# Kernel optimization log

Hardware: AMD Instinct MI355X
Metric: run time of the kernel (lower is better)

## Reference

```python
import jax, jax.numpy as jnp
import numpy as np

NUM_HEADS = 16

def setup_inputs() -> dict:
    key = jax.random.key(0)
    k1, k2, k3 = jax.random.split(key, 3)
    B, N, C = 4, 1024, 1024
    x = jax.random.normal(k1, (B, N, C), dtype=jnp.float32)
    w_qkv = jax.random.normal(k2, (C, 3 * C), dtype=jnp.float32) * (C ** -0.5)
    b_qkv = jnp.zeros((3 * C,), dtype=jnp.float32)
    w_proj = jax.random.normal(k3, (C, C), dtype=jnp.float32) * (C ** -0.5)
    b_proj = jnp.zeros((C,), dtype=jnp.float32)
    return {"x": x, "w_qkv": w_qkv, "b_qkv": b_qkv, "w_proj": w_proj, "b_proj": b_proj}

def reference(x, w_qkv, b_qkv, w_proj, b_proj):
    B, N, C = x.shape
    H = NUM_HEADS
    D = C // H
    scale = D ** -0.5
    # qkv projection: [B,N,3C] -> [3,B,H,N,D]
    qkv = (x @ w_qkv + b_qkv).reshape(B, N, 3, H, D).transpose(2, 0, 3, 1, 4)
    q, k, v = qkv[0], qkv[1], qkv[2]
    q = q * scale
    attn = jnp.einsum('bhnd,bhmd->bhnm', q, k)  # full N x N scores
    attn = jax.nn.softmax(attn, axis=-1)
    out = jnp.einsum('bhnm,bhmd->bhnd', attn, v)  # [B,H,N,D]
    out = out.transpose(0, 2, 1, 3).reshape(B, N, C)
    return out @ w_proj + b_proj
```

## Files before the change

kernel.cpp:

```cpp
#include <hip/hip_runtime.h>

typedef unsigned short u16;
typedef unsigned int u32;
typedef __attribute__((ext_vector_type(8))) short bf16x8;
typedef __attribute__((ext_vector_type(4))) float f32x4;
typedef __attribute__((ext_vector_type(16))) float f32x16;

#define LOG2E 1.4426950408889634f
#define QSCALE (0.125f * LOG2E)

__device__ __forceinline__ u16 f2bf(float f) {
  union { float f; u32 u; } x; x.f = f;
  u32 r = x.u + 0x7fffu + ((x.u >> 16) & 1u);
  return (u16)(r >> 16);
}

__device__ __forceinline__ u32 cvtpk(float a, float b) {
  u32 r;
  asm("v_cvt_pk_bf16_f32 %0, %1, %2" : "=v"(r) : "v"(a), "v"(b));
  return r;
}

__device__ __forceinline__ bf16x8 mkfrag(u32 a, u32 b, u32 c, u32 d) {
  union { u32 w[4]; bf16x8 v; } u;
  u.w[0] = a; u.w[1] = b; u.w[2] = c; u.w[3] = d;
  return u.v;
}

__device__ __forceinline__ void gload_lds16(const void* g, void* l) {
  __builtin_amdgcn_global_load_lds((const __attribute__((address_space(1))) u32*)g,
                                   (__attribute__((address_space(3))) u32*)l, 16, 0, 0);
}

__device__ __forceinline__ void packP(const f32x16& s, int hi, bf16x8& P0, bf16x8& P1) {
  u32 w0 = cvtpk(s[0], s[1]),  w1 = cvtpk(s[2], s[3]);
  u32 w2 = cvtpk(s[4], s[5]),  w3 = cvtpk(s[6], s[7]);
  u32 w4 = cvtpk(s[8], s[9]),  w5 = cvtpk(s[10], s[11]);
  u32 w6 = cvtpk(s[12], s[13]), w7 = cvtpk(s[14], s[15]);
  u32 x0 = __shfl_xor((int)w0, 32), x1 = __shfl_xor((int)w1, 32);
  u32 x2 = __shfl_xor((int)w2, 32), x3 = __shfl_xor((int)w3, 32);
  u32 x4 = __shfl_xor((int)w4, 32), x5 = __shfl_xor((int)w5, 32);
  u32 x6 = __shfl_xor((int)w6, 32), x7 = __shfl_xor((int)w7, 32);
  P0 = mkfrag(hi ? x2 : w0, hi ? x3 : w1, hi ? w2 : x0, hi ? w3 : x1);
  P1 = mkfrag(hi ? x6 : w4, hi ? x7 : w5, hi ? w6 : x4, hi ? w7 : x5);
}

__global__ __launch_bounds__(256) void k_cvt_x(const float* __restrict__ in, u16* __restrict__ out) {
  int i = blockIdx.x * 256 + threadIdx.x;
  const float4* p = (const float4*)in;
  float4 a = p[i * 2], b = p[i * 2 + 1];
  uint4 o;
  o.x = (u32)f2bf(a.x) | ((u32)f2bf(a.y) << 16);
  o.y = (u32)f2bf(a.z) | ((u32)f2bf(a.w) << 16);
  o.z = (u32)f2bf(b.x) | ((u32)f2bf(b.y) << 16);
  o.w = (u32)f2bf(b.z) | ((u32)f2bf(b.w) << 16);
  ((uint4*)out)[i] = o;
}

__global__ __launch_bounds__(256) void k_transpose_cvt(const float* __restrict__ src, u16* __restrict__ dst,
                                                       int R, int Cc) {
  __shared__ float tile[32][33];
  int c0 = blockIdx.x * 32, r0 = blockIdx.y * 32;
  int tx = threadIdx.x, ty = threadIdx.y;
  #pragma unroll
  for (int j = 0; j < 4; ++j)
    tile[ty * 4 + j][tx] = src[(r0 + ty * 4 + j) * Cc + c0 + tx];
  __syncthreads();
  #pragma unroll
  for (int j = 0; j < 4; ++j) {
    int cl = ty * 4 + j;
    dst[(c0 + cl) * R + r0 + tx] = f2bf(tile[tx][cl]);
  }
}

template <int EPI, int NBN>
__global__ __launch_bounds__(512) void k_gemm(const u16* __restrict__ A, const u16* __restrict__ Bt,
                                              const float* __restrict__ bias,
                                              u16* __restrict__ oq, u16* __restrict__ ok,
                                              u16* __restrict__ ovt, float* __restrict__ of) {
  __shared__ u16 lds[24576];
  const int tid = threadIdx.x;
  const int l = tid & 63, w = tid >> 6;
  const int wm = w >> 2, wn = w & 3;
  const int lr = l & 15, lh = l >> 4;
  const int cpx = gridDim.x >> 3;
  const int wg = (blockIdx.x & 7) * cpx + (blockIdx.x >> 3);
  const int bn = wg % NBN, bm = wg / NBN;

  f32x4 acc[4][2] = {};
  const int e = tid * 8;
  const int srow = e >> 5;
  const int sgr  = (e >> 3) & 3;
  const int scol = (sgr ^ ((srow >> 1) & 3)) * 8;
  const u16* gA = A + (bm * 128 + srow) * 1024 + scol;
  const u16* gB = Bt + (bn * 128 + srow) * 1024 + scol;

  #define GSTAGE(kk, b)                                              \
    do {                                                             \
      gload_lds16(gA + (kk), lds + (b) * 8192 + e);                  \
      gload_lds16(gB + (kk), lds + (b) * 8192 + 4096 + e);           \
    } while (0)

  GSTAGE(0, 0);
  GSTAGE(32, 1);
  int cur = 0, nxt = 2;

  for (int it = 0; it < 32; ++it) {
    if (it < 31) asm volatile("s_waitcnt vmcnt(2)" ::: "memory");
    else         asm volatile("s_waitcnt vmcnt(0)" ::: "memory");
    __builtin_amdgcn_s_barrier();
    __builtin_amdgcn_sched_barrier(0);

    if (it < 30) GSTAGE((it + 2) * 32, nxt);

    const u16* Asc = lds + cur * 8192;
    bf16x8 af[4], bfr[2];
    #pragma unroll
    for (int mi = 0; mi < 4; ++mi) {
      int r = wm * 64 + mi * 16 + lr;
      af[mi] = *(const bf16x8*)(Asc + r * 32 + ((lh ^ ((r >> 1) & 3)) * 8));
    }
    #pragma unroll
    for (int ni = 0; ni < 2; ++ni) {
      int r = wn * 32 + ni * 16 + lr;
      bfr[ni] = *(const bf16x8*)(Asc + 4096 + r * 32 + ((lh ^ ((r >> 1) & 3)) * 8));
    }
    #pragma unroll
    for (int mi = 0; mi < 4; ++mi)
      #pragma unroll
      for (int ni = 0; ni < 2; ++ni)
        acc[mi][ni] = __builtin_amdgcn_mfma_f32_16x16x32_bf16(af[mi], bfr[ni], acc[mi][ni], 0, 0, 0);

    cur = (cur == 2) ? 0 : cur + 1;
    nxt = (nxt == 2) ? 0 : nxt + 1;
  }
  #undef GSTAGE

  if (EPI == 0) {
    #pragma unroll
    for (int ni = 0; ni < 2; ++ni) {
      int col = bn * 128 + wn * 32 + ni * 16 + lr;
      float bb = bias[col];
      #pragma unroll
      for (int mi = 0; mi < 4; ++mi) {
        int row = bm * 128 + wm * 64 + mi * 16 + lh * 4;
        #pragma unroll
        for (int r = 0; r < 4; ++r)
          of[(row + r) * (NBN * 128) + col] = acc[mi][ni][r] + bb;
      }
    }
  } else {
    const int s = bn >> 3;
    __syncthreads();
    if (s < 2) {
      u16* dst = (s == 0) ? oq : ok;
      const float sc = (s == 0) ? QSCALE : 1.0f;
      #pragma unroll
      for (int ni = 0; ni < 2; ++ni) {
        int cl = wn * 32 + ni * 16 + lr;
        float bb = bias[bn * 128 + cl];
        #pragma unroll
        for (int mi = 0; mi < 4; ++mi) {
          int rl = wm * 64 + mi * 16 + lh * 4;
          #pragma unroll
          for (int r = 0; r < 4; ++r)
            lds[(rl + r) * 136 + cl] = f2bf((acc[mi][ni][r] + bb) * sc);
        }
      }
      __syncthreads();
      const int row = tid >> 2, q4 = tid & 3;
      const int h0 = ((bn * 128) & 1023) >> 6;
      const int b = (bm * 128) >> 10, n0 = (bm * 128) & 1023;
      const u16* srow2 = lds + row * 136 + q4 * 32;
      u16* drow = dst + ((u32)((b * 16 + h0 + (q4 >> 1)) * 1024) + n0 + row) * 64 + (q4 & 1) * 32;
      #pragma unroll
      for (int j = 0; j < 4; ++j)
        *(uint4*)(drow + j * 8) = *(const uint4*)(srow2 + j * 8);
    } else {
      #pragma unroll
      for (int ni = 0; ni < 2; ++ni) {
        int cl = wn * 32 + ni * 16 + lr;
        float bb = bias[bn * 128 + cl];
        #pragma unroll
        for (int mi = 0; mi < 4; ++mi) {
          int rl = wm * 64 + mi * 16 + lh * 4;
          u32 p0 = (u32)f2bf(acc[mi][ni][0] + bb) | ((u32)f2bf(acc[mi][ni][1] + bb) << 16);
          u32 p1 = (u32)f2bf(acc[mi][ni][2] + bb) | ((u32)f2bf(acc[mi][ni][3] + bb) << 16);
          uint2 pk; pk.x = p0; pk.y = p1;
          *(uint2*)(lds + cl * 136 + rl) = pk;
        }
      }
      __syncthreads();
      const int cl = tid >> 2, q4 = tid & 3;
      const int c = bn * 128 + cl, cc = c & 1023, h = cc >> 6, d = cc & 63;
      const int b = (bm * 128) >> 10, n0 = (bm * 128) & 1023;
      const u16* srow2 = lds + cl * 136 + q4 * 32;
      u16* drow = ovt + ((b * 16 + h) * 64 + d) * 1024 + n0 + q4 * 32;
      #pragma unroll
      for (int j = 0; j < 4; ++j)
        *(uint4*)(drow + j * 8) = *(const uint4*)(srow2 + j * 8);
    }
  }
}

__global__ __launch_bounds__(512) void k_attn(const u16* __restrict__ q, const u16* __restrict__ k,
                                              const u16* __restrict__ vt, u16* __restrict__ ao) {
  __shared__ u16 lds[40960];
  const int tid = threadIdx.x, l = tid & 63, w = tid >> 6;
  const int lq = l & 31, hi = l >> 5;
  const int g = w >> 2, wl = w & 3;
  const int i = blockIdx.x;
  const int bh = (i & 7) * 8 + ((i >> 3) & 7);
  const int qb = i >> 6;
  const int t0 = g * 8;

  const int qrow = qb * 128 + wl * 32 + lq;
  const u16* qg = q + bh * 65536 + qrow * 64;
  bf16x8 qf[4];
  #pragma unroll
  for (int ks = 0; ks < 4; ++ks)
    qf[ks] = *(const bf16x8*)(qg + ks * 16 + hi * 8);

  float lsum = 0.f;
  f32x16 o0 = {}, o1 = {};
  bf16x8 pa[4];

  const u16* kg = k + bh * 65536;
  const u16* vg = vt + bh * 65536;

  u16* Kl = lds + g * 8192;
  u16* Vl = lds + 16384 + g * 12288;

  const int tg = tid & 255;
  const int ch0 = tg, ch1 = 256 + tg;
  const int r0_ = ch0 >> 3, s0_ = (ch0 & 7) ^ (r0_ & 7);
  const int r1_ = ch1 >> 3, s1_ = (ch1 & 7) ^ (r1_ & 7);

  #define STAGE(t, kb, vb)                                                         \
    do {                                                                           \
      gload_lds16(kg + (t) * 4096 + r0_ * 64 + s0_ * 8, Kl + (kb) * 4096 + ch0 * 8); \
      gload_lds16(kg + (t) * 4096 + r1_ * 64 + s1_ * 8, Kl + (kb) * 4096 + ch1 * 8); \
      gload_lds16(vg + r0_ * 1024 + (t) * 64 + s0_ * 8, Vl + (vb) * 4096 + ch0 * 8); \
      gload_lds16(vg + r1_ * 1024 + (t) * 64 + s1_ * 8, Vl + (vb) * 4096 + ch1 * 8); \
    } while (0)

  const int swz = (lq & 7) << 4;

  #define QKM(kb, SA, SB)                                                      \
    do {                                                                       \
      const char* Kb = (const char*)(Kl + (kb) * 4096);                        \
      _Pragma("unroll")                                                        \
      for (int ks2 = 0; ks2 < 4; ++ks2) {                                      \
        bf16x8 kf0 = *(const bf16x8*)(Kb + (((lq) * 128 + ks2 * 32 + hi * 16) ^ swz));      \
        bf16x8 kf1 = *(const bf16x8*)(Kb + (((32 + lq) * 128 + ks2 * 32 + hi * 16) ^ swz)); \
        SA = __builtin_amdgcn_mfma_f32_32x32x16_bf16(kf0, qf[ks2], SA, 0, 0, 0); \
        SB = __builtin_amdgcn_mfma_f32_32x32x16_bf16(kf1, qf[ks2], SB, 0, 0, 0); \
      }                                                                        \
    } while (0)

  #define SM(SA, SB)                                                           \
    do {                                                                       \
      float l0 = 0.f, l1 = 0.f, l2 = 0.f, l3 = 0.f;                            \
      _Pragma("unroll") for (int r = 0; r < 16; r += 4) {                      \
        float e0 = __builtin_amdgcn_exp2f(SA[r]);                              \
        float e1 = __builtin_amdgcn_exp2f(SA[r + 1]);                          \
        float e2 = __builtin_amdgcn_exp2f(SA[r + 2]);                          \
        float e3 = __builtin_amdgcn_exp2f(SA[r + 3]);                          \
        SA[r] = e0; SA[r + 1] = e1; SA[r + 2] = e2; SA[r + 3] = e3;            \
        l0 += e0; l1 += e1; l2 += e2; l3 += e3;                                \
      }                                                                        \
      _Pragma("unroll") for (int r = 0; r < 16; r += 4) {                      \
        float e0 = __builtin_amdgcn_exp2f(SB[r]);                              \
        float e1 = __builtin_amdgcn_exp2f(SB[r + 1]);                          \
        float e2 = __builtin_amdgcn_exp2f(SB[r + 2]);                          \
        float e3 = __builtin_amdgcn_exp2f(SB[r + 3]);                          \
        SB[r] = e0; SB[r + 1] = e1; SB[r + 2] = e2; SB[r + 3] = e3;            \
        l0 += e0; l1 += e1; l2 += e2; l3 += e3;                                \
      }                                                                        \
      lsum += (l0 + l1) + (l2 + l3);                                           \
      packP(SA, hi, pa[0], pa[1]);                                             \
      packP(SB, hi, pa[2], pa[3]);                                             \
    } while (0)

  #define PVM(vb)                                                              \
    do {                                                                       \
      const char* Vb = (const char*)(Vl + (vb) * 4096);                        \
      _Pragma("unroll")                                                        \
      for (int ks2 = 0; ks2 < 4; ++ks2) {                                      \
        bf16x8 vf0 = *(const bf16x8*)(Vb + (((lq) * 128 + ks2 * 32 + hi * 16) ^ swz));      \
        bf16x8 vf1 = *(const bf16x8*)(Vb + (((32 + lq) * 128 + ks2 * 32 + hi * 16) ^ swz)); \
        o0 = __builtin_amdgcn_mfma_f32_32x32x16_bf16(pa[ks2], vf0, o0, 0, 0, 0); \
        o1 = __builtin_amdgcn_mfma_f32_32x32x16_bf16(pa[ks2], vf1, o1, 0, 0, 0); \
      }                                                                        \
    } while (0)

  STAGE(t0, 0, 0);
  STAGE(t0 + 1, 1, 1);

  asm volatile("s_waitcnt vmcnt(6)" ::: "memory");
  __builtin_amdgcn_s_barrier();
  __builtin_amdgcn_sched_barrier(0);
  {
    f32x16 sA = {}, sB = {};
    QKM(0, sA, sB);
    SM(sA, sB);
  }

  for (int tl = 0; tl < 7; ++tl) {
    const int vb = tl % 3;
    const int kb1 = (tl + 1) & 1;
    if (tl < 6) asm volatile("s_waitcnt vmcnt(2)" ::: "memory");
    else        asm volatile("s_waitcnt vmcnt(0)" ::: "memory");
    __builtin_amdgcn_s_barrier();
    __builtin_amdgcn_sched_barrier(0);
    if (tl < 6) STAGE(t0 + tl + 2, (tl + 2) & 1, (tl + 2) % 3);

    f32x16 sA = {}, sB = {};
    __builtin_amdgcn_s_setprio(1);
    PVM(vb);
    QKM(kb1, sA, sB);
    __builtin_amdgcn_s_setprio(0);
    SM(sA, sB);
  }
  PVM(1);
  #undef STAGE
  #undef QKM
  #undef SM
  #undef PVM

  lsum += __shfl_xor(lsum, 32);

  __syncthreads();
  float* mf = (float*)lds;
  const int mbase = (wl * 64 + l) * 33;
  if (g == 1) {
    #pragma unroll
    for (int r = 0; r < 16; ++r) { mf[mbase + r] = o0[r]; mf[mbase + 16 + r] = o1[r]; }
    mf[8448 + wl * 64 + l] = lsum;
  }
  __syncthreads();
  if (g == 0) {
    #pragma unroll
    for (int r = 0; r < 16; ++r) { o0[r] += mf[mbase + r]; o1[r] += mf[mbase + 16 + r]; }
    lsum += mf[8448 + wl * 64 + l];

    const int b = bh >> 4, h = bh & 15;
    u16* aob = ao + (u32)(b * 1024 + qb * 128 + wl * 32) * 1024 + h * 64;
    #pragma unroll
    for (int r = 0; r < 16; ++r) {
      int row = (r & 3) + 8 * (r >> 2) + 4 * hi;
      float inv = 1.0f / __shfl(lsum, row, 64);
      aob[row * 1024 + lq]      = f2bf(o0[r] * inv);
      aob[row * 1024 + 32 + lq] = f2bf(o1[r] * inv);
    }
  }
}

extern "C" void kernel_launch(void* const* d_in, const int* in_sizes, int n_in,
                              void* d_out, int out_size, void* d_ws, size_t ws_size,
                              hipStream_t stream) {
  const float* x      = (const float*)d_in[0];
  const float* w_qkv  = (const float*)d_in[1];
  const float* b_qkv  = (const float*)d_in[2];
  const float* w_proj = (const float*)d_in[3];
  const float* b_proj = (const float*)d_in[4];
  float* out = (float*)d_out;
  char* ws = (char*)d_ws;

  u16* X16   = (u16*)ws;
  u16* Wqkv  = (u16*)(ws + 8388608);
  u16* Wproj = (u16*)(ws + 14680064);
  u16* Q     = (u16*)(ws + 16777216);
  u16* K     = (u16*)(ws + 25165824);
  u16* VT    = (u16*)(ws + 33554432);
  u16* AO    = X16;

  k_cvt_x<<<dim3(2048), dim3(256), 0, stream>>>(x, X16);
  k_transpose_cvt<<<dim3(96, 32), dim3(32, 8), 0, stream>>>(w_qkv, Wqkv, 1024, 3072);
  k_transpose_cvt<<<dim3(32, 32), dim3(32, 8), 0, stream>>>(w_proj, Wproj, 1024, 1024);
  k_gemm<1, 24><<<dim3(768), dim3(512), 0, stream>>>(X16, Wqkv, b_qkv, Q, K, VT, (float*)0);
  k_attn<<<dim3(512), dim3(512), 0, stream>>>(Q, K, VT, AO);
  k_gemm<0, 8><<<dim3(256), dim3(512), 0, stream>>>(AO, Wproj, b_proj, (u16*)0, (u16*)0, (u16*)0, out);
}
```

Before: 99.50 us.

## Replace QKV GEMM with 256x256-tile kernel using phased LDS pipeline

Adds a dedicated QKV projection GEMM that uses 256x256 output tiles with a double-buffered 128 KB LDS layout, XOR-swizzled reads, and eight interleaved load/compute phases per iteration with setprio and explicit waitcnts. The launch drops from 768 to 192 blocks and the epilogue writes Q/K/V^T in four 128x128 quadrants through LDS. It aims to raise arithmetic intensity and overlap global loads with MFMA work. In exchange, 192 blocks underfill a 256-CU device and the kernel carries heavy register and LDS pressure.

```diff
diff --git a/kernel.cpp b/kernel.cpp
--- a/kernel.cpp
+++ b/kernel.cpp
@@ -73,6 +73,161 @@
   }
 }
 
+__global__ __launch_bounds__(512, 2) void k_gemm256(const u16* __restrict__ A, const u16* __restrict__ Bt,
+                                                    const float* __restrict__ bias,
+                                                    u16* __restrict__ oq, u16* __restrict__ ok,
+                                                    u16* __restrict__ ovt) {
+  __shared__ u16 lds[65536];
+  const int tid = threadIdx.x;
+  const int l = tid & 63, w = tid >> 6;
+  const int wm = w >> 2, wn = w & 3;
+  const int lr = l & 15, lh = l >> 4;
+  const int cpx = gridDim.x >> 3;
+  const int wg = (blockIdx.x & 7) * cpx + (blockIdx.x >> 3);
+  const int bn = wg % 12, bm = wg / 12;
+
+  f32x4 acc[8][4] = {};
+
+  const int sg0 = (tid & 7) ^ ((tid >> 3) & 7);
+  const u16* aB = A  + (bm * 256 + (tid >> 3)) * 1024 + sg0 * 8;
+  const u16* bB = Bt + (bn * 256 + (tid >> 3)) * 1024 + sg0 * 8;
+
+  const int key = (lr & 7) << 4;
+  const int cB0 = (lh * 16) ^ key;
+  const int cB1 = (64 + lh * 16) ^ key;
+  const int arow0 = wm * 64 + lr;
+  const int brow0 = wn * 32 + lr;
+
+  #define STA(h, kt, buf) do {                                                          \
+    gload_lds16(aB + ((h) * 128) * 1024 + (kt) * 64, lds + (buf) * 16384 + (h) * 8192 + tid * 8);        \
+    gload_lds16(aB + ((h) * 128 + 64) * 1024 + (kt) * 64, lds + (buf) * 16384 + (h) * 8192 + 4096 + tid * 8); \
+  } while (0)
+  #define STB(h, kt, buf) do {                                                          \
+    gload_lds16(bB + ((h) * 128) * 1024 + (kt) * 64, lds + 32768 + (buf) * 16384 + (h) * 8192 + tid * 8);        \
+    gload_lds16(bB + ((h) * 128 + 64) * 1024 + (kt) * 64, lds + 32768 + (buf) * 16384 + (h) * 8192 + 4096 + tid * 8); \
+  } while (0)
+
+  #define PHASE(buf, mh, nh, STAGE_STMT, FENCE_STMT)                                    \
+  {                                                                                     \
+    const u16* Ab = lds + (buf) * 16384 + (mh) * 8192;                                  \
+    const u16* Bb = lds + 32768 + (buf) * 16384 + (nh) * 8192;                          \
+    bf16x8 a_[4][2], b_[2][2];                                                          \
+    _Pragma("unroll") for (int m2 = 0; m2 < 4; ++m2) {                                  \
+      int rb = (arow0 + m2 * 16) * 128;                                                 \
+      a_[m2][0] = *(const bf16x8*)((const char*)Ab + rb + cB0);                         \
+      a_[m2][1] = *(const bf16x8*)((const char*)Ab + rb + cB1);                         \
+    }                                                                                   \
+    _Pragma("unroll") for (int n2 = 0; n2 < 2; ++n2) {                                  \
+      int rb = (brow0 + n2 * 16) * 128;                                                 \
+      b_[n2][0] = *(const bf16x8*)((const char*)Bb + rb + cB0);                         \
+      b_[n2][1] = *(const bf16x8*)((const char*)Bb + rb + cB1);                         \
+    }                                                                                   \
+    STAGE_STMT;                                                                         \
+    __builtin_amdgcn_s_barrier();                                                       \
+    asm volatile("s_waitcnt lgkmcnt(0)" ::: "memory");                                  \
+    __builtin_amdgcn_sched_barrier(0);                                                  \
+    __builtin_amdgcn_s_setprio(1);                                                      \
+    _Pragma("unroll") for (int m2 = 0; m2 < 4; ++m2)                                    \
+      _Pragma("unroll") for (int n2 = 0; n2 < 2; ++n2) {                                \
+        acc[(mh) * 4 + m2][(nh) * 2 + n2] = __builtin_amdgcn_mfma_f32_16x16x32_bf16(    \
+            a_[m2][0], b_[n2][0], acc[(mh) * 4 + m2][(nh) * 2 + n2], 0, 0, 0);          \
+        acc[(mh) * 4 + m2][(nh) * 2 + n2] = __builtin_amdgcn_mfma_f32_16x16x32_bf16(    \
+            a_[m2][1], b_[n2][1], acc[(mh) * 4 + m2][(nh) * 2 + n2], 0, 0, 0);          \
+      }                                                                                 \
+    __builtin_amdgcn_s_setprio(0);                                                      \
+    FENCE_STMT;                                                                         \
+    __builtin_amdgcn_s_barrier();                                                       \
+    __builtin_amdgcn_sched_barrier(0);                                                  \
+  }
+
+  STA(0, 0, 0); STB(1, 0, 0); STA(1, 0, 0); STB(0, 0, 0);
+  STA(0, 1, 1); STB(1, 1, 1);
+  asm volatile("s_waitcnt vmcnt(4)" ::: "memory");
+  __builtin_amdgcn_s_barrier();
+  __builtin_amdgcn_sched_barrier(0);
+
+  for (int it = 0; it < 8; ++it) {
+    const int kt1 = 2 * it + 1, ktA = 2 * it + 2, ktB = 2 * it + 3;
+    const bool more = (it < 7);
+    PHASE(0, 0, 0, { STA(1, kt1, 1); }, {});
+    PHASE(0, 0, 1, { STB(0, kt1, 1); }, {});
+    PHASE(0, 1, 1, { if (more) STA(0, ktA, 0); }, {});
+    PHASE(0, 1, 0, { if (more) STB(1, ktA, 0); },
+          { if (more) asm volatile("s_waitcnt vmcnt(4)" ::: "memory");
+            else      asm volatile("s_waitcnt vmcnt(0)" ::: "memory"); });
+    PHASE(1, 0, 0, { if (more) STA(1, ktA, 0); }, {});
+    PHASE(1, 0, 1, { if (more) STB(0, ktA, 0); }, {});
+    PHASE(1, 1, 1, { if (more) STA(0, ktB, 1); }, {});
+    PHASE(1, 1, 0, { if (more) STB(1, ktB, 1); },
+          { if (more) asm volatile("s_waitcnt vmcnt(4)" ::: "memory");
+            else      asm volatile("s_waitcnt vmcnt(0)" ::: "memory"); });
+  }
+  #undef PHASE
+  #undef STA
+  #undef STB
+
+  const int s = bn >> 2;
+  const int row = tid >> 2, q4 = tid & 3;
+  if (s < 2) {
+    u16* dst = s ? ok : oq;
+    const float sc = s ? 1.0f : QSCALE;
+    #pragma unroll
+    for (int qr = 0; qr < 4; ++qr) {
+      const int rh = qr >> 1, chh = qr & 1;
+      __syncthreads();
+      #pragma unroll
+      for (int m2 = 0; m2 < 4; ++m2)
+        #pragma unroll
+        for (int n2 = 0; n2 < 2; ++n2) {
+          f32x4 av = acc[rh * 4 + m2][chh * 2 + n2];
+          int cl = wn * 32 + n2 * 16 + lr;
+          float bb = bias[bn * 256 + chh * 128 + cl];
+          int rl = wm * 64 + m2 * 16 + lh * 4;
+          #pragma unroll
+          for (int r = 0; r < 4; ++r)
+            lds[(rl + r) * 136 + cl] = f2bf((av[r] + bb) * sc);
+        }
+      __syncthreads();
+      int m = bm * 256 + rh * 128 + row;
+      int b = m >> 10, n = m & 1023;
+      int h0 = ((bn * 256 + chh * 128) & 1023) >> 6;
+      const u16* srow2 = lds + row * 136 + q4 * 32;
+      u16* drow = dst + ((u32)((b * 16 + h0 + (q4 >> 1)) * 1024) + n) * 64 + (q4 & 1) * 32;
+      #pragma unroll
+      for (int j = 0; j < 4; ++j)
+        *(uint4*)(drow + j * 8) = *(const uint4*)(srow2 + j * 8);
+    }
+  } else {
+    #pragma unroll
+    for (int qr = 0; qr < 4; ++qr) {
+      const int rh = qr >> 1, chh = qr & 1;
+      __syncthreads();
+      #pragma unroll
+      for (int m2 = 0; m2 < 4; ++m2)
+        #pragma unroll
+        for (int n2 = 0; n2 < 2; ++n2) {
+          f32x4 av = acc[rh * 4 + m2][chh * 2 + n2];
+          int cl = wn * 32 + n2 * 16 + lr;
+          float bb = bias[bn * 256 + chh * 128 + cl];
+          int rl = wm * 64 + m2 * 16 + lh * 4;
+          u32 p0 = (u32)f2bf(av[0] + bb) | ((u32)f2bf(av[1] + bb) << 16);
+          u32 p1 = (u32)f2bf(av[2] + bb) | ((u32)f2bf(av[3] + bb) << 16);
+          uint2 pk; pk.x = p0; pk.y = p1;
+          *(uint2*)(lds + cl * 136 + rl) = pk;
+        }
+      __syncthreads();
+      int c = bn * 256 + chh * 128 + row;
+      int cc = c & 1023, h = cc >> 6, d = cc & 63;
+      int b = (bm * 256) >> 10, n0 = (bm * 256 + rh * 128) & 1023;
+      const u16* srow2 = lds + row * 136 + q4 * 32;
+      u16* drow = ovt + ((b * 16 + h) * 64 + d) * 1024 + n0 + q4 * 32;
+      #pragma unroll
+      for (int j = 0; j < 4; ++j)
+        *(uint4*)(drow + j * 8) = *(const uint4*)(srow2 + j * 8);
+    }
+  }
+}
+
 template <int EPI, int NBN>
 __global__ __launch_bounds__(512) void k_gemm(const u16* __restrict__ A, const u16* __restrict__ Bt,
                                               const float* __restrict__ bias,
@@ -148,57 +303,6 @@
         for (int r = 0; r < 4; ++r)
           of[(row + r) * (NBN * 128) + col] = acc[mi][ni][r] + bb;
       }
-    }
-  } else {
-    const int s = bn >> 3;
-    __syncthreads();
-    if (s < 2) {
-      u16* dst = (s == 0) ? oq : ok;
-      const float sc = (s == 0) ? QSCALE : 1.0f;
-      #pragma unroll
-      for (int ni = 0; ni < 2; ++ni) {
-        int cl = wn * 32 + ni * 16 + lr;
-        float bb = bias[bn * 128 + cl];
-        #pragma unroll
-        for (int mi = 0; mi < 4; ++mi) {
-          int rl = wm * 64 + mi * 16 + lh * 4;
-          #pragma unroll
-          for (int r = 0; r < 4; ++r)
-            lds[(rl + r) * 136 + cl] = f2bf((acc[mi][ni][r] + bb) * sc);
-        }
-      }
-      __syncthreads();
-      const int row = tid >> 2, q4 = tid & 3;
-      const int h0 = ((bn * 128) & 1023) >> 6;
-      const int b = (bm * 128) >> 10, n0 = (bm * 128) & 1023;
-      const u16* srow2 = lds + row * 136 + q4 * 32;
-      u16* drow = dst + ((u32)((b * 16 + h0 + (q4 >> 1)) * 1024) + n0 + row) * 64 + (q4 & 1) * 32;
-      #pragma unroll
-      for (int j = 0; j < 4; ++j)
-        *(uint4*)(drow + j * 8) = *(const uint4*)(srow2 + j * 8);
-    } else {
-      #pragma unroll
-      for (int ni = 0; ni < 2; ++ni) {
-        int cl = wn * 32 + ni * 16 + lr;
-        float bb = bias[bn * 128 + cl];
-        #pragma unroll
-        for (int mi = 0; mi < 4; ++mi) {
-          int rl = wm * 64 + mi * 16 + lh * 4;
-          u32 p0 = (u32)f2bf(acc[mi][ni][0] + bb) | ((u32)f2bf(acc[mi][ni][1] + bb) << 16);
-          u32 p1 = (u32)f2bf(acc[mi][ni][2] + bb) | ((u32)f2bf(acc[mi][ni][3] + bb) << 16);
-          uint2 pk; pk.x = p0; pk.y = p1;
-          *(uint2*)(lds + cl * 136 + rl) = pk;
-        }
-      }
-      __syncthreads();
-      const int cl = tid >> 2, q4 = tid & 3;
-      const int c = bn * 128 + cl, cc = c & 1023, h = cc >> 6, d = cc & 63;
-      const int b = (bm * 128) >> 10, n0 = (bm * 128) & 1023;
-      const u16* srow2 = lds + cl * 136 + q4 * 32;
-      u16* drow = ovt + ((b * 16 + h) * 64 + d) * 1024 + n0 + q4 * 32;
-      #pragma unroll
-      for (int j = 0; j < 4; ++j)
-        *(uint4*)(drow + j * 8) = *(const uint4*)(srow2 + j * 8);
     }
   }
 }
@@ -378,7 +482,7 @@
   k_cvt_x<<<dim3(2048), dim3(256), 0, stream>>>(x, X16);
   k_transpose_cvt<<<dim3(96, 32), dim3(32, 8), 0, stream>>>(w_qkv, Wqkv, 1024, 3072);
   k_transpose_cvt<<<dim3(32, 32), dim3(32, 8), 0, stream>>>(w_proj, Wproj, 1024, 1024);
-  k_gemm<1, 24><<<dim3(768), dim3(512), 0, stream>>>(X16, Wqkv, b_qkv, Q, K, VT, (float*)0);
+  k_gemm256<<<dim3(192), dim3(512), 0, stream>>>(X16, Wqkv, b_qkv, Q, K, VT);
   k_attn<<<dim3(512), dim3(512), 0, stream>>>(Q, K, VT, AO);
   k_gemm<0, 8><<<dim3(256), dim3(512), 0, stream>>>(AO, Wproj, b_proj, (u16*)0, (u16*)0, (u16*)0, out);
 }
```

New measurement: 104.6 us. 5.1% more time.
